# Performance work log

Measured on AMD Instinct MI355X. Metric: run time of the kernel, lower is better.

The kernel has to match this reference:

```python
import jax, jax.numpy as jnp
from jax import lax
import numpy as np

B, N, D = 8, 4096, 64
S = 1024          # groups
K = 32            # kneighbors
RADIUS = 0.2


def farthest_point_sample(xyz, npoint):
    """xyz: [B,N,3] -> centroid indices [B,npoint]. Deterministic start at index 0
    (original torch uses a random start index)."""
    b, n, _ = xyz.shape

    def step(carry, _):
        distance, farthest = carry                              # [B,N], [B]
        centroid = jnp.take_along_axis(xyz, farthest[:, None, None], axis=1)  # [B,1,3]
        dist = jnp.sum((xyz - centroid) ** 2, axis=-1)          # [B,N]
        distance = jnp.minimum(distance, dist)
        new_far = jnp.argmax(distance, axis=-1)
        return (distance, new_far), farthest

    init = (jnp.full((b, n), 1e10, xyz.dtype), jnp.zeros((b,), jnp.int32))
    _, cents = lax.scan(step, init, None, length=npoint)        # [npoint,B]
    return cents.T                                              # [B,npoint]


def square_distance(src, dst):
    # [B,N,M] squared euclidean distances
    d = -2.0 * jnp.einsum('bnc,bmc->bnm', src, dst)
    d += jnp.sum(src ** 2, -1)[:, :, None]
    d += jnp.sum(dst ** 2, -1)[:, None, :]
    return d


def query_ball_point(radius, nsample, xyz, new_xyz):
    b, n, _ = xyz.shape
    s = new_xyz.shape[1]
    sqrdists = square_distance(new_xyz, xyz)                    # [B,S,N]
    arange = jnp.arange(n, dtype=jnp.int32)[None, None, :]
    group_idx = jnp.where(sqrdists > radius ** 2, n, arange)    # [B,S,N]
    group_idx = jnp.sort(group_idx, axis=-1)[:, :, :nsample]    # [B,S,K]
    first = group_idx[:, :, :1]
    group_idx = jnp.where(group_idx == n, first, group_idx)
    return group_idx


def gather_points(points, idx):
    # points [B,N,C], idx [B,...] -> [B,...,C]
    return jax.vmap(lambda p, i: p[i])(points, idx)


def setup_inputs() -> dict:
    key = jax.random.key(0)
    k1, k2 = jax.random.split(key)
    xyz = jax.random.uniform(k1, (B, N, 3), dtype=jnp.float32)
    points = jax.random.normal(k2, (B, N, D), dtype=jnp.float32)
    return {"xyz": xyz, "points": points}


def reference(xyz, points):
    fps_idx = farthest_point_sample(xyz, S)                     # [B,S]
    new_xyz = gather_points(xyz, fps_idx)                       # [B,S,3]
    anchor_feat = gather_points(points, fps_idx)                # [B,S,D]
    idx = query_ball_point(RADIUS, K, xyz, new_xyz)             # [B,S,K]
    grouped_xyz = gather_points(xyz, idx)                       # [B,S,K,3]
    grouped_points = gather_points(points, idx)                 # [B,S,K,D]
    grouped_points = jnp.concatenate([grouped_points, grouped_xyz], axis=-1)  # use_xyz
    anchor_rep = jnp.broadcast_to(anchor_feat[:, :, None, :], (B, S, K, D))
    new_points = jnp.concatenate([grouped_points, anchor_rep], axis=-1)  # [B,S,K,2D+3]
    return new_xyz, new_points
```

## Files before the change

kernel.cpp:

```cpp
#include <hip/hip_runtime.h>

#define BB 8
#define NN 4096
#define DD 64
#define SS 1024
#define KK 32
#define R2 0.04f

typedef float f32x2 __attribute__((ext_vector_type(2)));

#define DPP_MAXF(wv, CTRL)                                                             \
    {                                                                                  \
        int _o = __builtin_amdgcn_update_dpp(__float_as_int(wv), __float_as_int(wv),   \
                                             CTRL, 0xf, 0xf, false);                   \
        (wv) = fmaxf((wv), __int_as_float(_o));                                        \
    }

#define XCH2(CTRL)                                                                     \
    {                                                                                  \
        const unsigned o_lo = (unsigned)__builtin_amdgcn_update_dpp(                   \
            (int)r_lo, (int)r_lo, CTRL, 0xf, 0xf, false);                              \
        const unsigned o_hi = (unsigned)__builtin_amdgcn_update_dpp(                   \
            (int)r_hi, (int)r_hi, CTRL, 0xf, 0xf, false);                              \
        const unsigned long long _m = ((unsigned long long)r_hi << 32) | r_lo;         \
        const unsigned long long _o = ((unsigned long long)o_hi << 32) | o_lo;         \
        const bool _tk = _o > _m;                                                      \
        r_lo = _tk ? o_lo : r_lo;                                                      \
        r_hi = _tk ? o_hi : r_hi;                                                      \
    }

__global__ __launch_bounds__(512) void fused_kernel(const float* __restrict__ xyz,
                                                    const float* __restrict__ points,
                                                    float* __restrict__ out) {
#pragma clang fp contract(off)
    __shared__ float4 sxyz[NN];
    __shared__ unsigned long long lpad[1408];
    __shared__ int sfar[SS];
    __shared__ int bbuf[8][KK];
    __shared__ unsigned long long wrec8[2][8];

    const int tid  = threadIdx.x;
    const int wave = tid >> 6;
    const int lane = tid & 63;
    const int b    = blockIdx.x >> 5;
    const int cs   = blockIdx.x & 31;
    const float* xb = xyz + (size_t)b * NN * 3;
    const float* pb = points + (size_t)b * NN * DD;

    for (int i = tid; i < 1408; i += 512) lpad[i] = 0ull;

    const float4* xb4 = (const float4*)(xb + tid * 24);
    const float4 q0 = xb4[0], q1 = xb4[1], q2 = xb4[2];
    const float4 q3 = xb4[3], q4 = xb4[4], q5 = xb4[5];

    f32x2 px[4], py[4], pz[4], dist[4];
    px[0] = (f32x2){q0.x, q0.w}; py[0] = (f32x2){q0.y, q1.x}; pz[0] = (f32x2){q0.z, q1.y};
    px[1] = (f32x2){q1.z, q2.y}; py[1] = (f32x2){q1.w, q2.z}; pz[1] = (f32x2){q2.x, q2.w};
    px[2] = (f32x2){q3.x, q3.w}; py[2] = (f32x2){q3.y, q4.x}; pz[2] = (f32x2){q3.z, q4.y};
    px[3] = (f32x2){q4.z, q5.y}; py[3] = (f32x2){q4.w, q5.z}; pz[3] = (f32x2){q5.x, q5.w};
#pragma unroll
    for (int jj = 0; jj < 4; ++jj) {
        const int i0 = tid * 8 + 2 * jj;
        sxyz[i0]     = make_float4(px[jj].x, py[jj].x, pz[jj].x, 0.0f);
        sxyz[i0 + 1] = make_float4(px[jj].y, py[jj].y, pz[jj].y, 0.0f);
        dist[jj] = (f32x2){1e10f, 1e10f};
    }
    __syncthreads();

    int far = (int)(unsigned)lpad[0];

    const int tmax = cs * 32 + 32;
    for (int t = 0; t < tmax; ++t) {
        if (tid == 0) sfar[t] = far;
        const float4 c = sxyz[far];
        const f32x2 cx2 = (f32x2){c.x, c.x}, cy2 = (f32x2){c.y, c.y},
                    cz2 = (f32x2){c.z, c.z};

        f32x2 nd[4];
#pragma unroll
        for (int jj = 0; jj < 4; ++jj) {
            const f32x2 dx = px[jj] - cx2;
            const f32x2 dy = py[jj] - cy2;
            const f32x2 dz = pz[jj] - cz2;
            const f32x2 d  = (dx * dx + dy * dy) + dz * dz;
            f32x2 m;
            m.x = fminf(dist[jj].x, d.x);
            m.y = fminf(dist[jj].y, d.y);
            dist[jj] = m;
            nd[jj] = m;
        }
        const float t0 = fmaxf(fmaxf(nd[0].x, nd[0].y), nd[1].x);
        const float t1 = fmaxf(fmaxf(nd[1].y, nd[2].x), nd[2].y);
        const float t2 = fmaxf(nd[3].x, nd[3].y);
        const float bestv = fmaxf(fmaxf(t0, t1), t2);
        int localj = 0;
#pragma unroll
        for (int j = 7; j >= 0; --j) {
            const float v = (j & 1) ? nd[j >> 1].y : nd[j >> 1].x;
            if (v == bestv) localj = j;
        }

        float wv = bestv;
        DPP_MAXF(wv, 0x111);
        DPP_MAXF(wv, 0x112);
        DPP_MAXF(wv, 0x114);
        DPP_MAXF(wv, 0x118);
        DPP_MAXF(wv, 0x142);
        DPP_MAXF(wv, 0x143);
        const float maxw =
            __int_as_float(__builtin_amdgcn_readlane(__float_as_int(wv), 63));

        const unsigned long long hits = __ballot(bestv == maxw);
        const int L = __ffsll(hits) - 1;
        if (lane == L) {
            wrec8[t & 1][wave] =
                ((unsigned long long)__float_as_uint(bestv) << 32) |
                (unsigned)~(unsigned)(tid * 8 + localj);
        }
        __syncthreads();

        const unsigned long long k8 = wrec8[t & 1][lane & 7];
        unsigned r_lo = (unsigned)k8, r_hi = (unsigned)(k8 >> 32);
        XCH2(0xB1);
        XCH2(0x4E);
        XCH2(0x141);
        far = (int)~r_lo;
    }

#pragma unroll
    for (int i = 0; i < 4; ++i) {
        const int s  = cs * 32 + wave * 4 + i;
        const int g  = b * SS + s;
        const int qi = sfar[s];
        const float4 q = sxyz[qi];
        const float qn = __fadd_rn(__fadd_rn(__fmul_rn(q.x, q.x), __fmul_rn(q.y, q.y)),
                                   __fmul_rn(q.z, q.z));

        int total = 0;
        for (int base = 0; base < NN && total < KK; base += 64) {
            const int n = base + lane;
            const float4 p = sxyz[n];
            const float pn = __fadd_rn(__fadd_rn(__fmul_rn(p.x, p.x), __fmul_rn(p.y, p.y)),
                                       __fmul_rn(p.z, p.z));
            const float dt = __fadd_rn(__fadd_rn(__fmul_rn(q.x, p.x), __fmul_rn(q.y, p.y)),
                                       __fmul_rn(q.z, p.z));
            const float d = __fadd_rn(__fadd_rn(__fmul_rn(-2.0f, dt), qn), pn);
            const bool hit = !(d > R2);
            const unsigned long long mask = __ballot(hit);
            const int before = __popcll(mask & ((1ull << lane) - 1ull));
            const int pos = total + before;
            if (hit && pos < KK) bbuf[wave][pos] = n;
            total += (int)__popcll(mask);
        }
        if (lane < KK) {
            const int v = (lane < total) ? bbuf[wave][lane] : bbuf[wave][0];
            bbuf[wave][lane] = v;
        }

        if (lane < 3)
            out[(size_t)g * 3 + lane] = (lane == 0) ? q.x : (lane == 1) ? q.y : q.z;

        const float a1 = (lane >= 3) ? pb[qi * DD + (lane - 3)] : 0.0f;
        const float a2 = (lane < 3) ? pb[qi * DD + (61 + lane)] : 0.0f;

        float* outp = out + (size_t)BB * SS * 3 + (size_t)g * (KK * 131);
        for (int k = 0; k < KK; ++k) {
            const int idx = bbuf[wave][k];
            const float4 pi = sxyz[idx];
            outp[k * 131 + lane] = pb[idx * DD + lane];
            const float v1 = (lane == 0) ? pi.x
                           : (lane == 1) ? pi.y
                           : (lane == 2) ? pi.z
                                         : a1;
            outp[k * 131 + 64 + lane] = v1;
            if (lane < 3) outp[k * 131 + 128 + lane] = a2;
        }
    }
}

extern "C" void kernel_launch(void* const* d_in, const int* in_sizes, int n_in,
                              void* d_out, int out_size, void* d_ws, size_t ws_size,
                              hipStream_t stream) {
    const float* xyz    = (const float*)d_in[0];
    const float* points = (const float*)d_in[1];
    float* out = (float*)d_out;

    fused_kernel<<<BB * 32, 512, 0, stream>>>(xyz, points, out);
}
```

Measured before the change: 829.8 us.

## Run FPS on four waves with 16 points per thread and LDS atomicMax reduction

The farthest-point-sampling loop now runs on 256 threads (four waves), each holding 16 points instead of 8, while the other four waves only match the barriers. The cross-wave argmax moves from a per-wave record array plus a DPP exchange to a 64-bit atomicMax into a per-iteration slot in shared memory, read back after the barrier. Points per thread are reloaded from shared memory rather than global registers. The aim is fewer participating waves in each barrier and a cheaper cross-wave reduction, at the cost of doubling the per-thread serial distance work and using LDS atomics.

```diff
diff --git a/kernel.cpp b/kernel.cpp
--- a/kernel.cpp
+++ b/kernel.cpp
@@ -16,28 +16,15 @@
         (wv) = fmaxf((wv), __int_as_float(_o));                                        \
     }
 
-#define XCH2(CTRL)                                                                     \
-    {                                                                                  \
-        const unsigned o_lo = (unsigned)__builtin_amdgcn_update_dpp(                   \
-            (int)r_lo, (int)r_lo, CTRL, 0xf, 0xf, false);                              \
-        const unsigned o_hi = (unsigned)__builtin_amdgcn_update_dpp(                   \
-            (int)r_hi, (int)r_hi, CTRL, 0xf, 0xf, false);                              \
-        const unsigned long long _m = ((unsigned long long)r_hi << 32) | r_lo;         \
-        const unsigned long long _o = ((unsigned long long)o_hi << 32) | o_lo;         \
-        const bool _tk = _o > _m;                                                      \
-        r_lo = _tk ? o_lo : r_lo;                                                      \
-        r_hi = _tk ? o_hi : r_hi;                                                      \
-    }
-
 __global__ __launch_bounds__(512) void fused_kernel(const float* __restrict__ xyz,
                                                     const float* __restrict__ points,
                                                     float* __restrict__ out) {
 #pragma clang fp contract(off)
     __shared__ float4 sxyz[NN];
-    __shared__ unsigned long long lpad[1408];
+    __shared__ unsigned long long red[SS];
     __shared__ int sfar[SS];
     __shared__ int bbuf[8][KK];
-    __shared__ unsigned long long wrec8[2][8];
+    __shared__ unsigned long long lpad[392];
 
     const int tid  = threadIdx.x;
     const int wave = tid >> 6;
@@ -47,84 +34,99 @@
     const float* xb = xyz + (size_t)b * NN * 3;
     const float* pb = points + (size_t)b * NN * DD;
 
-    for (int i = tid; i < 1408; i += 512) lpad[i] = 0ull;
+    for (int i = tid; i < SS; i += 512) red[i] = 0ull;
+    for (int i = tid; i < 392; i += 512) lpad[i] = 0ull;
 
-    const float4* xb4 = (const float4*)(xb + tid * 24);
-    const float4 q0 = xb4[0], q1 = xb4[1], q2 = xb4[2];
-    const float4 q3 = xb4[3], q4 = xb4[4], q5 = xb4[5];
-
-    f32x2 px[4], py[4], pz[4], dist[4];
-    px[0] = (f32x2){q0.x, q0.w}; py[0] = (f32x2){q0.y, q1.x}; pz[0] = (f32x2){q0.z, q1.y};
-    px[1] = (f32x2){q1.z, q2.y}; py[1] = (f32x2){q1.w, q2.z}; pz[1] = (f32x2){q2.x, q2.w};
-    px[2] = (f32x2){q3.x, q3.w}; py[2] = (f32x2){q3.y, q4.x}; pz[2] = (f32x2){q3.z, q4.y};
-    px[3] = (f32x2){q4.z, q5.y}; py[3] = (f32x2){q4.w, q5.z}; pz[3] = (f32x2){q5.x, q5.w};
+    {
+        const float4* xb4 = (const float4*)(xb + tid * 24);
+        const float4 q0 = xb4[0], q1 = xb4[1], q2 = xb4[2];
+        const float4 q3 = xb4[3], q4 = xb4[4], q5 = xb4[5];
+        float sx[8], sy[8], sz[8];
+        sx[0] = q0.x; sy[0] = q0.y; sz[0] = q0.z;
+        sx[1] = q0.w; sy[1] = q1.x; sz[1] = q1.y;
+        sx[2] = q1.z; sy[2] = q1.w; sz[2] = q2.x;
+        sx[3] = q2.y; sy[3] = q2.z; sz[3] = q2.w;
+        sx[4] = q3.x; sy[4] = q3.y; sz[4] = q3.z;
+        sx[5] = q3.w; sy[5] = q4.x; sz[5] = q4.y;
+        sx[6] = q4.z; sy[6] = q4.w; sz[6] = q5.x;
+        sx[7] = q5.y; sy[7] = q5.z; sz[7] = q5.w;
 #pragma unroll
-    for (int jj = 0; jj < 4; ++jj) {
-        const int i0 = tid * 8 + 2 * jj;
-        sxyz[i0]     = make_float4(px[jj].x, py[jj].x, pz[jj].x, 0.0f);
-        sxyz[i0 + 1] = make_float4(px[jj].y, py[jj].y, pz[jj].y, 0.0f);
-        dist[jj] = (f32x2){1e10f, 1e10f};
+        for (int j = 0; j < 8; ++j)
+            sxyz[tid * 8 + j] = make_float4(sx[j], sy[j], sz[j], 0.0f);
     }
     __syncthreads();
 
-    int far = (int)(unsigned)lpad[0];
+    const int tmax = cs * 32 + 32;
 
-    const int tmax = cs * 32 + 32;
-    for (int t = 0; t < tmax; ++t) {
-        if (tid == 0) sfar[t] = far;
-        const float4 c = sxyz[far];
-        const f32x2 cx2 = (f32x2){c.x, c.x}, cy2 = (f32x2){c.y, c.y},
-                    cz2 = (f32x2){c.z, c.z};
+    if (tid < 256) {
+        f32x2 px[8], py[8], pz[8], dist[8];
+#pragma unroll
+        for (int jj = 0; jj < 8; ++jj) {
+            const float4 p0 = sxyz[tid * 16 + 2 * jj];
+            const float4 p1 = sxyz[tid * 16 + 2 * jj + 1];
+            px[jj] = (f32x2){p0.x, p1.x};
+            py[jj] = (f32x2){p0.y, p1.y};
+            pz[jj] = (f32x2){p0.z, p1.z};
+            dist[jj] = (f32x2){1e10f, 1e10f};
+        }
+        int far = (int)(unsigned)lpad[0];
 
-        f32x2 nd[4];
+        for (int t = 0; t < tmax; ++t) {
+            if (tid == 0) sfar[t] = far;
+            const float4 c = sxyz[far];
+            const f32x2 cx2 = (f32x2){c.x, c.x}, cy2 = (f32x2){c.y, c.y},
+                        cz2 = (f32x2){c.z, c.z};
+
+            f32x2 nd[8];
 #pragma unroll
-        for (int jj = 0; jj < 4; ++jj) {
-            const f32x2 dx = px[jj] - cx2;
-            const f32x2 dy = py[jj] - cy2;
-            const f32x2 dz = pz[jj] - cz2;
-            const f32x2 d  = (dx * dx + dy * dy) + dz * dz;
-            f32x2 m;
-            m.x = fminf(dist[jj].x, d.x);
-            m.y = fminf(dist[jj].y, d.y);
-            dist[jj] = m;
-            nd[jj] = m;
+            for (int jj = 0; jj < 8; ++jj) {
+                const f32x2 dx = px[jj] - cx2;
+                const f32x2 dy = py[jj] - cy2;
+                const f32x2 dz = pz[jj] - cz2;
+                const f32x2 d  = (dx * dx + dy * dy) + dz * dz;
+                f32x2 m;
+                m.x = fminf(dist[jj].x, d.x);
+                m.y = fminf(dist[jj].y, d.y);
+                dist[jj] = m;
+                nd[jj] = m;
+            }
+            const float m0 = fmaxf(fmaxf(nd[0].x, nd[0].y), nd[1].x);
+            const float m1 = fmaxf(fmaxf(nd[1].y, nd[2].x), nd[2].y);
+            const float m2 = fmaxf(fmaxf(nd[3].x, nd[3].y), nd[4].x);
+            const float m3 = fmaxf(fmaxf(nd[4].y, nd[5].x), nd[5].y);
+            const float m4 = fmaxf(fmaxf(nd[6].x, nd[6].y), nd[7].x);
+            const float A  = fmaxf(fmaxf(m0, m1), m2);
+            const float B  = fmaxf(fmaxf(m3, m4), nd[7].y);
+            const float bestv = fmaxf(A, B);
+            int localj = 0;
+#pragma unroll
+            for (int j = 15; j >= 0; --j) {
+                const float v = (j & 1) ? nd[j >> 1].y : nd[j >> 1].x;
+                if (v == bestv) localj = j;
+            }
+
+            float wv = bestv;
+            DPP_MAXF(wv, 0x111);
+            DPP_MAXF(wv, 0x112);
+            DPP_MAXF(wv, 0x114);
+            DPP_MAXF(wv, 0x118);
+            DPP_MAXF(wv, 0x142);
+            DPP_MAXF(wv, 0x143);
+            const float maxw =
+                __int_as_float(__builtin_amdgcn_readlane(__float_as_int(wv), 63));
+
+            const unsigned long long hits = __ballot(bestv == maxw);
+            const int L = __ffsll(hits) - 1;
+            if (lane == L) {
+                atomicMax(&red[t],
+                          ((unsigned long long)__float_as_uint(bestv) << 32) |
+                              (unsigned)~(unsigned)(tid * 16 + localj));
+            }
+            __syncthreads();
+            far = (int)~(unsigned)red[t];
         }
-        const float t0 = fmaxf(fmaxf(nd[0].x, nd[0].y), nd[1].x);
-        const float t1 = fmaxf(fmaxf(nd[1].y, nd[2].x), nd[2].y);
-        const float t2 = fmaxf(nd[3].x, nd[3].y);
-        const float bestv = fmaxf(fmaxf(t0, t1), t2);
-        int localj = 0;
-#pragma unroll
-        for (int j = 7; j >= 0; --j) {
-            const float v = (j & 1) ? nd[j >> 1].y : nd[j >> 1].x;
-            if (v == bestv) localj = j;
-        }
-
-        float wv = bestv;
-        DPP_MAXF(wv, 0x111);
-        DPP_MAXF(wv, 0x112);
-        DPP_MAXF(wv, 0x114);
-        DPP_MAXF(wv, 0x118);
-        DPP_MAXF(wv, 0x142);
-        DPP_MAXF(wv, 0x143);
-        const float maxw =
-            __int_as_float(__builtin_amdgcn_readlane(__float_as_int(wv), 63));
-
-        const unsigned long long hits = __ballot(bestv == maxw);
-        const int L = __ffsll(hits) - 1;
-        if (lane == L) {
-            wrec8[t & 1][wave] =
-                ((unsigned long long)__float_as_uint(bestv) << 32) |
-                (unsigned)~(unsigned)(tid * 8 + localj);
-        }
-        __syncthreads();
-
-        const unsigned long long k8 = wrec8[t & 1][lane & 7];
-        unsigned r_lo = (unsigned)k8, r_hi = (unsigned)(k8 >> 32);
-        XCH2(0xB1);
-        XCH2(0x4E);
-        XCH2(0x141);
-        far = (int)~r_lo;
+    } else {
+        for (int t = 0; t < tmax; ++t) __syncthreads();
     }
 
 #pragma unroll
```

Result: slower. 853.8 us (+2.9%).
